# Optimization experiments

Hardware: AMD Instinct MI355X
Metric: run time of the kernel (lower is better)

## Reference

```python
import jax, jax.numpy as jnp
import numpy as np

EPS = 1e-5
ROPE_BASE = 10000.0


def _layernorm(x, g, b):
    mu = jnp.mean(x, axis=-1, keepdims=True)
    var = jnp.mean(jnp.square(x - mu), axis=-1, keepdims=True)
    return (x - mu) * jax.lax.rsqrt(var + EPS) * g + b


def _rope(q, k):
    # q, k: (B, T, H, D); rotate interleaved pairs along last dim, positions over T
    T, D = q.shape[1], q.shape[-1]
    half = D // 2
    inv_freq = ROPE_BASE ** (-jnp.arange(half, dtype=jnp.float32) / half)
    ang = jnp.arange(T, dtype=jnp.float32)[:, None] * inv_freq  # (T, half)
    cos = jnp.cos(ang)[None, :, None, :]
    sin = jnp.sin(ang)[None, :, None, :]

    def rot(x):
        xr, xi = x[..., 0::2], x[..., 1::2]
        yr = xr * cos - xi * sin
        yi = xr * sin + xi * cos
        return jnp.stack([yr, yi], axis=-1).reshape(x.shape)

    return rot(q), rot(k)


def setup_inputs() -> dict:
    key = jax.random.key(0)
    ks = jax.random.split(key, 5)
    E, F, B, T = 1024, 4096, 2, 2048
    s = 0.02
    return {
        "x": jax.random.normal(ks[0], (B, T, E), jnp.float32),
        "in_proj_w": jax.random.normal(ks[1], (3 * E, E), jnp.float32) * s,
        "out_proj_w": jax.random.normal(ks[2], (E, E), jnp.float32) * s,
        "ln1_g": jnp.ones((E,), jnp.float32),
        "ln1_b": jnp.zeros((E,), jnp.float32),
        "ln2_g": jnp.ones((E,), jnp.float32),
        "ln2_b": jnp.zeros((E,), jnp.float32),
        "w1": jax.random.normal(ks[3], (F, E), jnp.float32) * s,
        "w2": jax.random.normal(ks[4], (E, F), jnp.float32) * s,
        "context": 256,
    }


def reference(x, in_proj_w, out_proj_w, ln1_g, ln1_b, ln2_g, ln2_b, w1, w2, context):
    B, T, E = x.shape
    H = 16
    D = E // H

    # ---- self-attention block (pre-norm, residual) ----
    h = _layernorm(x, ln1_g, ln1_b)
    proj = h @ in_proj_w.T  # (B, T, 3E)
    qkv = proj.reshape(B, T, 3, H, D)
    q = qkv[:, :, 0]  # (B, T, H, D)
    k = qkv[:, :, 1]
    v = qkv[:, :, 2].transpose(0, 2, 1, 3)  # (B, H, T, D)
    q, k = _rope(q, k)
    q = q.transpose(0, 2, 1, 3)  # (B, H, T, D)
    k = k.transpose(0, 2, 1, 3)

    pos = jnp.arange(T)
    delta = pos[:, None] - pos[None, :]  # (T, T)
    mask = (delta >= 0) & (delta < context)

    scores = jnp.einsum("bhtd,bhsd->bhts", q, k) / jnp.sqrt(jnp.float32(D))
    scores = jnp.where(mask[None, None], scores, jnp.float32(-1e30))
    attn = jax.nn.softmax(scores, axis=-1)
    o = jnp.einsum("bhts,bhsd->bhtd", attn, v)
    o = o.transpose(0, 2, 1, 3).reshape(B, T, E)
    x = x + o @ out_proj_w.T

    # ---- FFN block (pre-norm, residual) ----
    h = _layernorm(x, ln2_g, ln2_b)
    update = jax.nn.gelu(h @ w1.T, approximate=False) @ w2.T
    return x + update
```

## Files before the change

### kernel.cpp

```cpp
#include <hip/hip_runtime.h>
#include <math.h>

#define B_BATCH 2
#define T_SEQ   2048
#define E_DIM   1024
#define H_HEADS 16
#define D_HEAD  64
#define F_DIM   4096
#define M_ROWS  (B_BATCH * T_SEQ)

typedef __attribute__((ext_vector_type(8))) short short8;
typedef __attribute__((ext_vector_type(4))) float floatx4;
typedef __attribute__((ext_vector_type(8))) unsigned short ushortx8;

typedef __attribute__((address_space(1))) const void global_cvoid;
typedef __attribute__((address_space(3))) void lds_void;

__device__ __forceinline__ unsigned short f2bf(float f) {
    unsigned u = __float_as_uint(f);
    u += 0x7fffu + ((u >> 16) & 1u);
    return (unsigned short)(u >> 16);
}
__device__ __forceinline__ float bf2f(unsigned short h) {
    return __uint_as_float(((unsigned)h) << 16);
}

__device__ __forceinline__ float gelu_f(float v) {
    const float u = v * (0.7978845608f + 0.0356774081f * v * v);
    const float e = __expf(2.0f * u);
    const float t = 1.0f - 2.0f / (e + 1.0f);
    return 0.5f * v * (1.0f + t);
}

__device__ __forceinline__ float waveReduceSum(float v) {
#pragma unroll
    for (int off = 32; off > 0; off >>= 1) v += __shfl_xor(v, off, 64);
    return v;
}

__global__ __launch_bounds__(256) void cvt_all_kernel(const float* __restrict__ ipw,
                                                      const float* __restrict__ opw,
                                                      const float* __restrict__ w1,
                                                      const float* __restrict__ w2,
                                                      unsigned short* __restrict__ wqkv,
                                                      unsigned short* __restrict__ wout,
                                                      unsigned short* __restrict__ w1b,
                                                      unsigned short* __restrict__ w2b) {
    const size_t MEG = 1024u * 1024u;
    size_t i = ((size_t)blockIdx.x * 256 + threadIdx.x) * 4;
    const float* src;
    unsigned short* dst;
    size_t off;
    if (i < 3 * MEG)      { src = ipw; dst = wqkv; off = i; }
    else if (i < 4 * MEG) { src = opw; dst = wout; off = i - 3 * MEG; }
    else if (i < 8 * MEG) { src = w1;  dst = w1b;  off = i - 4 * MEG; }
    else                  { src = w2;  dst = w2b;  off = i - 8 * MEG; }
    float4 v = *(const float4*)(src + off);
    ushort4 o;
    o.x = f2bf(v.x); o.y = f2bf(v.y); o.z = f2bf(v.z); o.w = f2bf(v.w);
    *(ushort4*)(dst + off) = o;
}

template <bool HASR>
__global__ __launch_bounds__(256) void reduce4_kernel(const unsigned short* __restrict__ p,
                                                      const float* __restrict__ R,
                                                      float* __restrict__ out, int n) {
    const int i = (blockIdx.x * 256 + threadIdx.x) * 8;
    if (i >= n) return;
    ushortx8 a0 = *(const ushortx8*)(p + i);
    ushortx8 a1 = *(const ushortx8*)(p + (size_t)n + i);
    ushortx8 a2 = *(const ushortx8*)(p + 2 * (size_t)n + i);
    ushortx8 a3 = *(const ushortx8*)(p + 3 * (size_t)n + i);
    float base[8];
    if (HASR) {
        float4 r0 = *(const float4*)(R + i);
        float4 r1 = *(const float4*)(R + i + 4);
        base[0]=r0.x; base[1]=r0.y; base[2]=r0.z; base[3]=r0.w;
        base[4]=r1.x; base[5]=r1.y; base[6]=r1.z; base[7]=r1.w;
    } else {
        float4 r0 = *(const float4*)(out + i);
        float4 r1 = *(const float4*)(out + i + 4);
        base[0]=r0.x; base[1]=r0.y; base[2]=r0.z; base[3]=r0.w;
        base[4]=r1.x; base[5]=r1.y; base[6]=r1.z; base[7]=r1.w;
    }
    float4 o0, o1;
    float* op = &o0.x;
#pragma unroll
    for (int j = 0; j < 8; ++j) {
        float s = base[j] + (bf2f(a0[j]) + bf2f(a1[j])) + (bf2f(a2[j]) + bf2f(a3[j]));
        if (j < 4) (&o0.x)[j] = s; else (&o1.x)[j - 4] = s;
    }
    (void)op;
    *(float4*)(out + i)     = o0;
    *(float4*)(out + i + 4) = o1;
}

__global__ __launch_bounds__(256) void rope_tab_kernel(float* __restrict__ tab) {
    const int idx = blockIdx.x * 256 + threadIdx.x;
    const int pos = idx >> 5, i = idx & 31;
    const float invf = powf(10000.0f, -(float)i / 32.0f);
    const float ang = (float)pos * invf;
    tab[idx * 2]     = cosf(ang);
    tab[idx * 2 + 1] = sinf(ang);
}

__global__ __launch_bounds__(256) void ln_kernel(const float* __restrict__ x,
                                                 const float* __restrict__ g,
                                                 const float* __restrict__ b,
                                                 unsigned short* __restrict__ out) {
    const int row = blockIdx.x;
    const float* xr = x + (size_t)row * E_DIM;
    float4 v = ((const float4*)xr)[threadIdx.x];
    float s  = v.x + v.y + v.z + v.w;
    float sq = v.x * v.x + v.y * v.y + v.z * v.z + v.w * v.w;

    __shared__ float red[8];
    float ws_ = waveReduceSum(s);
    float wq  = waveReduceSum(sq);
    int wid = threadIdx.x >> 6;
    if ((threadIdx.x & 63) == 0) { red[wid] = ws_; red[wid + 4] = wq; }
    __syncthreads();
    float ts = red[0] + red[1] + red[2] + red[3];
    float tq = red[4] + red[5] + red[6] + red[7];
    float mean = ts * (1.0f / E_DIM);
    float var  = tq * (1.0f / E_DIM) - mean * mean;
    float inv  = rsqrtf(var + 1e-5f);

    float4 gv = ((const float4*)g)[threadIdx.x];
    float4 bv = ((const float4*)b)[threadIdx.x];
    ushort4 o;
    o.x = f2bf((v.x - mean) * inv * gv.x + bv.x);
    o.y = f2bf((v.y - mean) * inv * gv.y + bv.y);
    o.z = f2bf((v.z - mean) * inv * gv.z + bv.z);
    o.w = f2bf((v.w - mean) * inv * gv.w + bv.w);
    ((ushort4*)(out + (size_t)row * E_DIM))[threadIdx.x] = o;
}

template <int EPI, int Z>
__global__ __launch_bounds__(256) void gemm_bf16(const unsigned short* __restrict__ A,
                                                 const unsigned short* __restrict__ Wt,
                                                 float* __restrict__ Cf,
                                                 unsigned short* __restrict__ Cb,
                                                 int M, int N, int K) {
    __shared__ unsigned short As[128 * 64];
    __shared__ unsigned short Bs[128 * 64];
    const int tid  = threadIdx.x;
    const int wave = tid >> 6, lane = tid & 63;
    const int wm   = wave >> 1, wn = wave & 1;
    const int quad = lane >> 4, l16 = lane & 15;

    const int id  = blockIdx.x;
    const int xcd = id & 7, local = id >> 3;
    const int mq  = M >> 9;
    const int mt  = (xcd & 3) + 4 * (local % mq);
    int nt_, zz;
    if (Z == 1) {
        zz  = 0;
        nt_ = (xcd >> 2) + 2 * (local / mq);
    } else {
        zz  = (xcd >> 2) + 2 * ((local / mq) & 1);
        nt_ = local / (mq * 2);
    }
    const int m0 = mt * 128, n0 = nt_ * 128;
    const int Kc = K / Z, kbeg = zz * Kc;

    const int row_rel = lane >> 3;
    const int ch      = lane & 7;

    const floatx4 z = {0.0f, 0.0f, 0.0f, 0.0f};
    floatx4 acc[4][4];
#pragma unroll
    for (int i = 0; i < 4; ++i)
#pragma unroll
        for (int j = 0; j < 4; ++j) acc[i][j] = z;

    for (int k0 = kbeg; k0 < kbeg + Kc; k0 += 64) {
        __syncthreads();
#pragma unroll
        for (int i = 0; i < 4; ++i) {
            const int chunk = wave * 4 + i;
            const int grow  = chunk * 8 + row_rel;
            const int lch   = ch ^ (grow & 7);
            const unsigned short* ga = A  + (size_t)(m0 + grow) * K + k0 + lch * 8;
            const unsigned short* gb = Wt + (size_t)(n0 + grow) * K + k0 + lch * 8;
            __builtin_amdgcn_global_load_lds((global_cvoid*)ga,
                                             (lds_void*)(As + chunk * 512), 16, 0, 0);
            __builtin_amdgcn_global_load_lds((global_cvoid*)gb,
                                             (lds_void*)(Bs + chunk * 512), 16, 0, 0);
        }
        __syncthreads();

#pragma unroll
        for (int ks = 0; ks < 2; ++ks) {
            short8 af[4], bfr[4];
#pragma unroll
            for (int mt2 = 0; mt2 < 4; ++mt2) {
                const int r = wm * 64 + mt2 * 16 + l16;
                const int p = (ks * 4 + quad) ^ (r & 7);
                af[mt2] = *(const short8*)(As + r * 64 + p * 8);
            }
#pragma unroll
            for (int nt2 = 0; nt2 < 4; ++nt2) {
                const int r = wn * 64 + nt2 * 16 + l16;
                const int p = (ks * 4 + quad) ^ (r & 7);
                bfr[nt2] = *(const short8*)(Bs + r * 64 + p * 8);
            }
#pragma unroll
            for (int mt2 = 0; mt2 < 4; ++mt2)
#pragma unroll
                for (int nt2 = 0; nt2 < 4; ++nt2)
                    acc[mt2][nt2] = __builtin_amdgcn_mfma_f32_16x16x32_bf16(
                        af[mt2], bfr[nt2], acc[mt2][nt2], 0, 0, 0);
        }
    }

    const size_t zoff = (size_t)zz * M * N;
#pragma unroll
    for (int mt2 = 0; mt2 < 4; ++mt2) {
        const int rb = m0 + wm * 64 + mt2 * 16 + quad * 4;
#pragma unroll
        for (int nt2 = 0; nt2 < 4; ++nt2) {
            const int col = n0 + wn * 64 + nt2 * 16 + l16;
#pragma unroll
            for (int r = 0; r < 4; ++r) {
                const size_t idx = (size_t)(rb + r) * N + col;
                const float v = acc[mt2][nt2][r];
                if (EPI == 2) {
                    Cb[idx] = f2bf(gelu_f(v));
                } else if (EPI == 4) {
                    Cb[idx] = f2bf(v);
                } else {
                    Cb[zoff + idx] = f2bf(v);
                }
            }
        }
    }
}

__global__ __launch_bounds__(256) void vtrans_kernel(const unsigned short* __restrict__ proj,
                                                     unsigned short* __restrict__ vt) {
    __shared__ unsigned short L[64 * 72];
    const int bh = blockIdx.y, b = bh >> 4, h = bh & 15;
    const int st = blockIdx.x * 64;
    const int tid = threadIdx.x;
    {
        const int srel = tid >> 2, d16 = (tid & 3) * 16;
        const unsigned short* src =
            proj + (size_t)(b * T_SEQ + st + srel) * (3 * E_DIM) + 2 * E_DIM + h * 64 + d16;
        *(short8*)(L + srel * 72 + d16)     = *(const short8*)(src);
        *(short8*)(L + srel * 72 + d16 + 8) = *(const short8*)(src + 8);
    }
    __syncthreads();
    {
        const int d = tid >> 2, s16 = (tid & 3) * 16;
        short8 o0, o1;
#pragma unroll
        for (int j = 0; j < 8; ++j) {
            o0[j] = (short)L[(s16 + j) * 72 + d];
            o1[j] = (short)L[(s16 + 8 + j) * 72 + d];
        }
        unsigned short* dst = vt + (size_t)(bh * 64 + d) * T_SEQ + st + s16;
        *(short8*)dst       = o0;
        *(short8*)(dst + 8) = o1;
    }
}

__device__ __forceinline__ void rope16(ushortx8 x0, ushortx8 x1, const float* tp,
                                       short8& y0, short8& y1) {
#pragma unroll
    for (int j = 0; j < 4; ++j) {
        const float c = tp[2 * j], s = tp[2 * j + 1];
        const float xr = bf2f(x0[2 * j]), xi = bf2f(x0[2 * j + 1]);
        y0[2 * j]     = (short)f2bf(xr * c - xi * s);
        y0[2 * j + 1] = (short)f2bf(xr * s + xi * c);
    }
#pragma unroll
    for (int j = 0; j < 4; ++j) {
        const float c = tp[8 + 2 * j], s = tp[8 + 2 * j + 1];
        const float xr = bf2f(x1[2 * j]), xi = bf2f(x1[2 * j + 1]);
        y1[2 * j]     = (short)f2bf(xr * c - xi * s);
        y1[2 * j + 1] = (short)f2bf(xr * s + xi * c);
    }
}

__global__ __launch_bounds__(256) void attn_kernel(const unsigned short* __restrict__ proj,
                                                   const unsigned short* __restrict__ vt,
                                                   const float* __restrict__ tab,
                                                   const int* __restrict__ ctxp,
                                                   unsigned short* __restrict__ o) {
    __shared__ unsigned short Qs[64 * 64];
    __shared__ unsigned short Ks[64 * 64];
    __shared__ unsigned short Vs[64 * 64];
    __shared__ unsigned short Ps[4][16 * 64];

    const int ctx = ctxp[0];
    const int tid = threadIdx.x;
    const int wave = tid >> 6, lane = tid & 63;
    const int quad = lane >> 4, l16 = lane & 15;
    const int bh = blockIdx.y, b = bh >> 4, h = bh & 15;
    const int t0 = blockIdx.x * 64;

    {
        const int r = tid >> 2, d16 = (tid & 3) * 16;
        const int pos = t0 + r;
        const unsigned short* src =
            proj + (size_t)(b * T_SEQ + pos) * (3 * E_DIM) + h * 64 + d16;
        ushortx8 x0 = *(const ushortx8*)src;
        ushortx8 x1 = *(const ushortx8*)(src + 8);
        const float* tp = tab + ((size_t)pos * 32 + (d16 >> 1)) * 2;
        short8 y0, y1;
        rope16(x0, x1, tp, y0, y1);
        const int c0 = (tid & 3) * 2;
        *(short8*)(Qs + r * 64 + ((c0)     ^ (r & 7)) * 8) = y0;
        *(short8*)(Qs + r * 64 + ((c0 + 1) ^ (r & 7)) * 8) = y1;
    }

    int first = t0 - (ctx - 1);
    if (first < 0) first = 0;
    const int first_base = first & ~63;

    float m[4] = {-1e30f, -1e30f, -1e30f, -1e30f};
    float l[4] = {0.0f, 0.0f, 0.0f, 0.0f};
    const floatx4 z = {0.0f, 0.0f, 0.0f, 0.0f};
    floatx4 accO[4] = {z, z, z, z};

    const int q_row0 = t0 + wave * 16 + quad * 4;

    for (int s_base = first_base; s_base <= t0; s_base += 64) {
        __syncthreads();
        {
            const int r = tid >> 2, d16 = (tid & 3) * 16;
            const int pos = s_base + r;
            const unsigned short* src =
                proj + (size_t)(b * T_SEQ + pos) * (3 * E_DIM) + E_DIM + h * 64 + d16;
            ushortx8 x0 = *(const ushortx8*)src;
            ushortx8 x1 = *(const ushortx8*)(src + 8);
            const float* tp = tab + ((size_t)pos * 32 + (d16 >> 1)) * 2;
            short8 y0, y1;
            rope16(x0, x1, tp, y0, y1);
            const int c0 = (tid & 3) * 2;
            *(short8*)(Ks + r * 64 + ((c0)     ^ (r & 7)) * 8) = y0;
            *(short8*)(Ks + r * 64 + ((c0 + 1) ^ (r & 7)) * 8) = y1;
        }
#pragma unroll
        for (int i = 0; i < 2; ++i) {
            const int chunk = (wave * 2 + i) * 64 + lane;
            const int d = chunk >> 3, c = chunk & 7;
            const unsigned short* gsrc =
                vt + (size_t)(bh * 64 + d) * T_SEQ + s_base + ((c ^ (d & 7)) * 8);
            __builtin_amdgcn_global_load_lds((global_cvoid*)gsrc,
                                             (lds_void*)(Vs + (wave * 2 + i) * 512),
                                             16, 0, 0);
        }
        __syncthreads();

        floatx4 accS[4] = {z, z, z, z};
#pragma unroll
        for (int ks = 0; ks < 2; ++ks) {
            const int qrow = wave * 16 + l16;
            short8 aq = *(const short8*)(Qs + qrow * 64 + (((ks * 4 + quad) ^ (qrow & 7)) * 8));
#pragma unroll
            for (int nt = 0; nt < 4; ++nt) {
                const int kro = nt * 16 + l16;
                short8 bk = *(const short8*)(Ks + kro * 64 + (((ks * 4 + quad) ^ (kro & 7)) * 8));
                accS[nt] = __builtin_amdgcn_mfma_f32_16x16x32_bf16(aq, bk, accS[nt], 0, 0, 0);
            }
        }

        float p[4][4];
        float alpha[4];
#pragma unroll
        for (int r = 0; r < 4; ++r) {
            const int qa = q_row0 + r;
            float sv[4];
            float vmax = -1e30f;
#pragma unroll
            for (int nt = 0; nt < 4; ++nt) {
                const int sa = s_base + nt * 16 + l16;
                const int dd = qa - sa;
                const bool ok = (unsigned)dd < (unsigned)ctx;
                const float s = ok ? accS[nt][r] * 0.125f : -1e30f;
                sv[nt] = s;
                vmax = fmaxf(vmax, s);
            }
            vmax = fmaxf(vmax, __shfl_xor(vmax, 1));
            vmax = fmaxf(vmax, __shfl_xor(vmax, 2));
            vmax = fmaxf(vmax, __shfl_xor(vmax, 4));
            vmax = fmaxf(vmax, __shfl_xor(vmax, 8));
            const float mn = fmaxf(m[r], vmax);
            alpha[r] = __expf(m[r] - mn);
            float ps = 0.0f;
#pragma unroll
            for (int nt = 0; nt < 4; ++nt) {
                const float pe = (sv[nt] > -0.5e30f) ? __expf(sv[nt] - mn) : 0.0f;
                p[nt][r] = pe;
                ps += pe;
            }
            ps += __shfl_xor(ps, 1);
            ps += __shfl_xor(ps, 2);
            ps += __shfl_xor(ps, 4);
            ps += __shfl_xor(ps, 8);
            l[r] = l[r] * alpha[r] + ps;
            m[r] = mn;
        }

#pragma unroll
        for (int nt = 0; nt < 4; ++nt) {
#pragma unroll
            for (int r = 0; r < 4; ++r) {
                const int row = quad * 4 + r;
                const int col = nt * 16 + l16;
                Ps[wave][row * 64 + (((col >> 3) ^ (row & 7)) * 8) + (col & 7)] =
                    f2bf(p[nt][r]);
            }
        }
#pragma unroll
        for (int nt = 0; nt < 4; ++nt)
#pragma unroll
            for (int r = 0; r < 4; ++r) accO[nt][r] *= alpha[r];

#pragma unroll
        for (int ks = 0; ks < 2; ++ks) {
            short8 ap = *(const short8*)(&Ps[wave][l16 * 64 + (((ks * 4 + quad) ^ (l16 & 7)) * 8)]);
#pragma unroll
            for (int nt = 0; nt < 4; ++nt) {
                const int dr = nt * 16 + l16;
                short8 bv = *(const short8*)(Vs + dr * 64 + (((ks * 4 + quad) ^ (dr & 7)) * 8));
                accO[nt] = __builtin_amdgcn_mfma_f32_16x16x32_bf16(ap, bv, accO[nt], 0, 0, 0);
            }
        }
    }

    float inv[4];
#pragma unroll
    for (int r = 0; r < 4; ++r) inv[r] = 1.0f / l[r];
#pragma unroll
    for (int nt = 0; nt < 4; ++nt) {
#pragma unroll
        for (int r = 0; r < 4; ++r) {
            const int t = q_row0 + r;
            o[(size_t)(b * T_SEQ + t) * E_DIM + h * 64 + nt * 16 + l16] =
                f2bf(accO[nt][r] * inv[r]);
        }
    }
}

extern "C" void kernel_launch(void* const* d_in, const int* in_sizes, int n_in,
                              void* d_out, int out_size, void* d_ws, size_t ws_size,
                              hipStream_t stream) {
    const float* x          = (const float*)d_in[0];
    const float* in_proj_w  = (const float*)d_in[1];
    const float* out_proj_w = (const float*)d_in[2];
    const float* ln1_g      = (const float*)d_in[3];
    const float* ln1_b      = (const float*)d_in[4];
    const float* ln2_g      = (const float*)d_in[5];
    const float* ln2_b      = (const float*)d_in[6];
    const float* w1         = (const float*)d_in[7];
    const float* w2         = (const float*)d_in[8];
    const int*   ctx        = (const int*)d_in[9];
    float* out = (float*)d_out;
    float* ws  = (float*)d_ws;

    const size_t MEG = 1024u * 1024u;
    unsigned short* u = (unsigned short*)ws;
    unsigned short* w2_b   = u;
    unsigned short* wqkv_b = u + 4 * MEG;
    unsigned short* wout_b = u + 7 * MEG;
    unsigned short* w1_b   = u + 8 * MEG;
    unsigned short* h_b    = u + 12 * MEG;
    unsigned short* obuf_b = u + 16 * MEG;
    unsigned short* proj_b = u + 20 * MEG;
    unsigned short* vt_b   = u + 32 * MEG;
    unsigned short* mid_b  = u + 36 * MEG;
    float* tab  = ws + 26 * MEG;
    unsigned short* part_op   = u + 20 * MEG;
    unsigned short* part_mlp2 = u + 4 * MEG;

    cvt_all_kernel<<<12 * MEG / 1024, 256, 0, stream>>>(
        in_proj_w, out_proj_w, w1, w2, wqkv_b, wout_b, w1_b, w2_b);
    rope_tab_kernel<<<T_SEQ * 32 / 256, 256, 0, stream>>>(tab);

    ln_kernel<<<M_ROWS, 256, 0, stream>>>(x, ln1_g, ln1_b, h_b);
    gemm_bf16<4, 1><<<32 * 24, 256, 0, stream>>>(
        h_b, wqkv_b, nullptr, proj_b, M_ROWS, 3 * E_DIM, E_DIM);
    vtrans_kernel<<<dim3(T_SEQ / 64, B_BATCH * H_HEADS), 256, 0, stream>>>(proj_b, vt_b);
    attn_kernel<<<dim3(T_SEQ / 64, B_BATCH * H_HEADS), 256, 0, stream>>>(
        proj_b, vt_b, tab, ctx, obuf_b);
    gemm_bf16<5, 4><<<32 * 8 * 4, 256, 0, stream>>>(
        obuf_b, wout_b, nullptr, part_op, M_ROWS, E_DIM, E_DIM);
    reduce4_kernel<true><<<M_ROWS * E_DIM / 2048, 256, 0, stream>>>(
        part_op, x, out, M_ROWS * E_DIM);
    ln_kernel<<<M_ROWS, 256, 0, stream>>>(out, ln2_g, ln2_b, h_b);
    gemm_bf16<2, 1><<<32 * 32, 256, 0, stream>>>(
        h_b, w1_b, nullptr, mid_b, M_ROWS, F_DIM, E_DIM);
    gemm_bf16<5, 4><<<32 * 8 * 4, 256, 0, stream>>>(
        mid_b, w2_b, nullptr, part_mlp2, M_ROWS, E_DIM, F_DIM);
    reduce4_kernel<false><<<M_ROWS * E_DIM / 2048, 256, 0, stream>>>(
        part_mlp2, nullptr, out, M_ROWS * E_DIM);
}
```

Baseline: 337.8 us.

## Fuse V transpose into QKV GEMM epilogue and residual-reduce into LayerNorm

```diff
diff --git a/kernel.cpp b/kernel.cpp
--- a/kernel.cpp
+++ b/kernel.cpp
@@ -61,40 +61,6 @@
     *(ushort4*)(dst + off) = o;
 }
 
-template <bool HASR>
-__global__ __launch_bounds__(256) void reduce4_kernel(const unsigned short* __restrict__ p,
-                                                      const float* __restrict__ R,
-                                                      float* __restrict__ out, int n) {
-    const int i = (blockIdx.x * 256 + threadIdx.x) * 8;
-    if (i >= n) return;
-    ushortx8 a0 = *(const ushortx8*)(p + i);
-    ushortx8 a1 = *(const ushortx8*)(p + (size_t)n + i);
-    ushortx8 a2 = *(const ushortx8*)(p + 2 * (size_t)n + i);
-    ushortx8 a3 = *(const ushortx8*)(p + 3 * (size_t)n + i);
-    float base[8];
-    if (HASR) {
-        float4 r0 = *(const float4*)(R + i);
-        float4 r1 = *(const float4*)(R + i + 4);
-        base[0]=r0.x; base[1]=r0.y; base[2]=r0.z; base[3]=r0.w;
-        base[4]=r1.x; base[5]=r1.y; base[6]=r1.z; base[7]=r1.w;
-    } else {
-        float4 r0 = *(const float4*)(out + i);
-        float4 r1 = *(const float4*)(out + i + 4);
-        base[0]=r0.x; base[1]=r0.y; base[2]=r0.z; base[3]=r0.w;
-        base[4]=r1.x; base[5]=r1.y; base[6]=r1.z; base[7]=r1.w;
-    }
-    float4 o0, o1;
-    float* op = &o0.x;
-#pragma unroll
-    for (int j = 0; j < 8; ++j) {
-        float s = base[j] + (bf2f(a0[j]) + bf2f(a1[j])) + (bf2f(a2[j]) + bf2f(a3[j]));
-        if (j < 4) (&o0.x)[j] = s; else (&o1.x)[j - 4] = s;
-    }
-    (void)op;
-    *(float4*)(out + i)     = o0;
-    *(float4*)(out + i + 4) = o1;
-}
-
 __global__ __launch_bounds__(256) void rope_tab_kernel(float* __restrict__ tab) {
     const int idx = blockIdx.x * 256 + threadIdx.x;
     const int pos = idx >> 5, i = idx & 31;
@@ -136,10 +102,187 @@
     ((ushort4*)(out + (size_t)row * E_DIM))[threadIdx.x] = o;
 }
 
+__global__ __launch_bounds__(256) void reduce_ln_kernel(const unsigned short* __restrict__ p,
+                                                        const float* __restrict__ x,
+                                                        const float* __restrict__ g,
+                                                        const float* __restrict__ bb,
+                                                        float* __restrict__ out,
+                                                        unsigned short* __restrict__ h) {
+    const int tid = threadIdx.x;
+    const int rh = tid >> 7;
+    const int l128 = tid & 127;
+    const int row = blockIdx.x * 2 + rh;
+    const size_t base = (size_t)row * E_DIM + l128 * 8;
+    const size_t n = (size_t)M_ROWS * E_DIM;
+
+    ushortx8 a0 = *(const ushortx8*)(p + base);
+    ushortx8 a1 = *(const ushortx8*)(p + n + base);
+    ushortx8 a2 = *(const ushortx8*)(p + 2 * n + base);
+    ushortx8 a3 = *(const ushortx8*)(p + 3 * n + base);
+    float4 r0 = *(const float4*)(x + base);
+    float4 r1 = *(const float4*)(x + base + 4);
+    float s[8] = {r0.x, r0.y, r0.z, r0.w, r1.x, r1.y, r1.z, r1.w};
+    float sum = 0.0f, sq = 0.0f;
+#pragma unroll
+    for (int j = 0; j < 8; ++j) {
+        s[j] += (bf2f(a0[j]) + bf2f(a1[j])) + (bf2f(a2[j]) + bf2f(a3[j]));
+        sum += s[j];
+        sq  += s[j] * s[j];
+    }
+    float4 o0 = {s[0], s[1], s[2], s[3]}, o1 = {s[4], s[5], s[6], s[7]};
+    *(float4*)(out + base)     = o0;
+    *(float4*)(out + base + 4) = o1;
+
+    sum = waveReduceSum(sum);
+    sq  = waveReduceSum(sq);
+    __shared__ float red[4][2];
+    const int wid = tid >> 6;
+    if ((tid & 63) == 0) { red[wid][0] = sum; red[wid][1] = sq; }
+    __syncthreads();
+    const float ts = red[rh * 2][0] + red[rh * 2 + 1][0];
+    const float tq = red[rh * 2][1] + red[rh * 2 + 1][1];
+    const float mean = ts * (1.0f / E_DIM);
+    const float var  = tq * (1.0f / E_DIM) - mean * mean;
+    const float inv  = rsqrtf(var + 1e-5f);
+
+    float4 g0 = *(const float4*)(g + l128 * 8);
+    float4 g1 = *(const float4*)(g + l128 * 8 + 4);
+    float4 b0 = *(const float4*)(bb + l128 * 8);
+    float4 b1 = *(const float4*)(bb + l128 * 8 + 4);
+    const float ga[8] = {g0.x, g0.y, g0.z, g0.w, g1.x, g1.y, g1.z, g1.w};
+    const float ba[8] = {b0.x, b0.y, b0.z, b0.w, b1.x, b1.y, b1.z, b1.w};
+    ushortx8 ho;
+#pragma unroll
+    for (int j = 0; j < 8; ++j) ho[j] = f2bf((s[j] - mean) * inv * ga[j] + ba[j]);
+    *(ushortx8*)(h + base) = ho;
+}
+
+__global__ __launch_bounds__(256) void reduce4_kernel(const unsigned short* __restrict__ p,
+                                                      float* __restrict__ out, int n) {
+    const int i = (blockIdx.x * 256 + threadIdx.x) * 8;
+    if (i >= n) return;
+    ushortx8 a0 = *(const ushortx8*)(p + i);
+    ushortx8 a1 = *(const ushortx8*)(p + (size_t)n + i);
+    ushortx8 a2 = *(const ushortx8*)(p + 2 * (size_t)n + i);
+    ushortx8 a3 = *(const ushortx8*)(p + 3 * (size_t)n + i);
+    float4 r0 = *(const float4*)(out + i);
+    float4 r1 = *(const float4*)(out + i + 4);
+    float s[8] = {r0.x, r0.y, r0.z, r0.w, r1.x, r1.y, r1.z, r1.w};
+#pragma unroll
+    for (int j = 0; j < 8; ++j)
+        s[j] += (bf2f(a0[j]) + bf2f(a1[j])) + (bf2f(a2[j]) + bf2f(a3[j]));
+    float4 o0 = {s[0], s[1], s[2], s[3]}, o1 = {s[4], s[5], s[6], s[7]};
+    *(float4*)(out + i)     = o0;
+    *(float4*)(out + i + 4) = o1;
+}
+
+__global__ __launch_bounds__(256) void gemm_qkv(const unsigned short* __restrict__ A,
+                                                const unsigned short* __restrict__ Wt,
+                                                unsigned short* __restrict__ proj,
+                                                unsigned short* __restrict__ vt) {
+    __shared__ unsigned short As[128 * 64];
+    __shared__ unsigned short Bs[128 * 64];
+    const int tid  = threadIdx.x;
+    const int wave = tid >> 6, lane = tid & 63;
+    const int wm   = wave >> 1, wn = wave & 1;
+    const int quad = lane >> 4, l16 = lane & 15;
+    const int M = M_ROWS, N = 3 * E_DIM, K = E_DIM;
+
+    const int id  = blockIdx.x;
+    const int xcd = id & 7, local = id >> 3;
+    const int mq  = M >> 9;
+    const int mt  = (xcd & 3) + 4 * (local % mq);
+    const int nt_ = (xcd >> 2) + 2 * (local / mq);
+    const int m0 = mt * 128, n0 = nt_ * 128;
+
+    const int row_rel = lane >> 3;
+    const int ch      = lane & 7;
+
+    const floatx4 z = {0.0f, 0.0f, 0.0f, 0.0f};
+    floatx4 acc[4][4];
+#pragma unroll
+    for (int i = 0; i < 4; ++i)
+#pragma unroll
+        for (int j = 0; j < 4; ++j) acc[i][j] = z;
+
+    for (int k0 = 0; k0 < K; k0 += 64) {
+        __syncthreads();
+#pragma unroll
+        for (int i = 0; i < 4; ++i) {
+            const int chunk = wave * 4 + i;
+            const int grow  = chunk * 8 + row_rel;
+            const int lch   = ch ^ (grow & 7);
+            const unsigned short* ga = A  + (size_t)(m0 + grow) * K + k0 + lch * 8;
+            const unsigned short* gb = Wt + (size_t)(n0 + grow) * K + k0 + lch * 8;
+            __builtin_amdgcn_global_load_lds((global_cvoid*)ga,
+                                             (lds_void*)(As + chunk * 512), 16, 0, 0);
+            __builtin_amdgcn_global_load_lds((global_cvoid*)gb,
+                                             (lds_void*)(Bs + chunk * 512), 16, 0, 0);
+        }
+        __syncthreads();
+
+#pragma unroll
+        for (int ks = 0; ks < 2; ++ks) {
+            short8 af[4], bfr[4];
+#pragma unroll
+            for (int mt2 = 0; mt2 < 4; ++mt2) {
+                const int r = wm * 64 + mt2 * 16 + l16;
+                const int p = (ks * 4 + quad) ^ (r & 7);
+                af[mt2] = *(const short8*)(As + r * 64 + p * 8);
+            }
+#pragma unroll
+            for (int nt2 = 0; nt2 < 4; ++nt2) {
+                const int r = wn * 64 + nt2 * 16 + l16;
+                const int p = (ks * 4 + quad) ^ (r & 7);
+                bfr[nt2] = *(const short8*)(Bs + r * 64 + p * 8);
+            }
+#pragma unroll
+            for (int mt2 = 0; mt2 < 4; ++mt2)
+#pragma unroll
+                for (int nt2 = 0; nt2 < 4; ++nt2)
+                    acc[mt2][nt2] = __builtin_amdgcn_mfma_f32_16x16x32_bf16(
+                        af[mt2], bfr[nt2], acc[mt2][nt2], 0, 0, 0);
+        }
+    }
+
+    const int type = n0 >> 10;
+    if (type < 2) {
+#pragma unroll
+        for (int mt2 = 0; mt2 < 4; ++mt2) {
+            const int rb = m0 + wm * 64 + mt2 * 16 + quad * 4;
+#pragma unroll
+            for (int nt2 = 0; nt2 < 4; ++nt2) {
+                const int col = n0 + wn * 64 + nt2 * 16 + l16;
+#pragma unroll
+                for (int r = 0; r < 4; ++r)
+                    proj[(size_t)(rb + r) * N + col] = f2bf(acc[mt2][nt2][r]);
+            }
+        }
+    } else {
+#pragma unroll
+        for (int mt2 = 0; mt2 < 4; ++mt2) {
+            const int rb = m0 + wm * 64 + mt2 * 16 + quad * 4;
+            const int t = rb & (T_SEQ - 1);
+            const int b = rb >> 11;
+#pragma unroll
+            for (int nt2 = 0; nt2 < 4; ++nt2) {
+                const int col = n0 + wn * 64 + nt2 * 16 + l16;
+                const int hh = (col - 2048) >> 6;
+                const int d  = col & 63;
+                ushort4 pk;
+                pk.x = f2bf(acc[mt2][nt2][0]);
+                pk.y = f2bf(acc[mt2][nt2][1]);
+                pk.z = f2bf(acc[mt2][nt2][2]);
+                pk.w = f2bf(acc[mt2][nt2][3]);
+                *(ushort4*)(vt + (((size_t)(b * H_HEADS + hh) * 64) + d) * T_SEQ + t) = pk;
+            }
+        }
+    }
+}
+
 template <int EPI, int Z>
 __global__ __launch_bounds__(256) void gemm_bf16(const unsigned short* __restrict__ A,
                                                  const unsigned short* __restrict__ Wt,
-                                                 float* __restrict__ Cf,
                                                  unsigned short* __restrict__ Cb,
                                                  int M, int N, int K) {
     __shared__ unsigned short As[128 * 64];
@@ -227,41 +370,11 @@
                 const float v = acc[mt2][nt2][r];
                 if (EPI == 2) {
                     Cb[idx] = f2bf(gelu_f(v));
-                } else if (EPI == 4) {
-                    Cb[idx] = f2bf(v);
                 } else {
                     Cb[zoff + idx] = f2bf(v);
                 }
             }
         }
-    }
-}
-
-__global__ __launch_bounds__(256) void vtrans_kernel(const unsigned short* __restrict__ proj,
-                                                     unsigned short* __restrict__ vt) {
-    __shared__ unsigned short L[64 * 72];
-    const int bh = blockIdx.y, b = bh >> 4, h = bh & 15;
-    const int st = blockIdx.x * 64;
-    const int tid = threadIdx.x;
-    {
-        const int srel = tid >> 2, d16 = (tid & 3) * 16;
-        const unsigned short* src =
-            proj + (size_t)(b * T_SEQ + st + srel) * (3 * E_DIM) + 2 * E_DIM + h * 64 + d16;
-        *(short8*)(L + srel * 72 + d16)     = *(const short8*)(src);
-        *(short8*)(L + srel * 72 + d16 + 8) = *(const short8*)(src + 8);
-    }
-    __syncthreads();
-    {
-        const int d = tid >> 2, s16 = (tid & 3) * 16;
-        short8 o0, o1;
-#pragma unroll
-        for (int j = 0; j < 8; ++j) {
-            o0[j] = (short)L[(s16 + j) * 72 + d];
-            o1[j] = (short)L[(s16 + 8 + j) * 72 + d];
-        }
-        unsigned short* dst = vt + (size_t)(bh * 64 + d) * T_SEQ + st + s16;
-        *(short8*)dst       = o0;
-        *(short8*)(dst + 8) = o1;
     }
 }
 
@@ -349,8 +462,7 @@
             const unsigned short* gsrc =
                 vt + (size_t)(bh * 64 + d) * T_SEQ + s_base + ((c ^ (d & 7)) * 8);
             __builtin_amdgcn_global_load_lds((global_cvoid*)gsrc,
-                                             (lds_void*)(Vs + (wave * 2 + i) * 512),
-                                             16, 0, 0);
+                                             (lds_void*)(Vs + (wave * 2 + i) * 512), 16, 0, 0);
         }
         __syncthreads();
 
@@ -472,7 +584,7 @@
     unsigned short* proj_b = u + 20 * MEG;
     unsigned short* vt_b   = u + 32 * MEG;
     unsigned short* mid_b  = u + 36 * MEG;
-    float* tab  = ws + 26 * MEG;
+    float* tab = ws + 26 * MEG;
     unsigned short* part_op   = u + 20 * MEG;
     unsigned short* part_mlp2 = u + 4 * MEG;
 
@@ -481,20 +593,17 @@
     rope_tab_kernel<<<T_SEQ * 32 / 256, 256, 0, stream>>>(tab);
 
     ln_kernel<<<M_ROWS, 256, 0, stream>>>(x, ln1_g, ln1_b, h_b);
-    gemm_bf16<4, 1><<<32 * 24, 256, 0, stream>>>(
-        h_b, wqkv_b, nullptr, proj_b, M_ROWS, 3 * E_DIM, E_DIM);
-    vtrans_kernel<<<dim3(T_SEQ / 64, B_BATCH * H_HEADS), 256, 0, stream>>>(proj_b, vt_b);
+    gemm_qkv<<<32 * 24, 256, 0, stream>>>(h_b, wqkv_b, proj_b, vt_b);
     attn_kernel<<<dim3(T_SEQ / 64, B_BATCH * H_HEADS), 256, 0, stream>>>(
         proj_b, vt_b, tab, ctx, obuf_b);
     gemm_bf16<5, 4><<<32 * 8 * 4, 256, 0, stream>>>(
-        obuf_b, wout_b, nullptr, part_op, M_ROWS, E_DIM, E_DIM);
-    reduce4_kernel<true><<<M_ROWS * E_DIM / 2048, 256, 0, stream>>>(
-        part_op, x, out, M_ROWS * E_DIM);
-    ln_kernel<<<M_ROWS, 256, 0, stream>>>(out, ln2_g, ln2_b, h_b);
+        obuf_b, wout_b, part_op, M_ROWS, E_DIM, E_DIM);
+    reduce_ln_kernel<<<M_ROWS / 2, 256, 0, stream>>>(
+        part_op, x, ln2_g, ln2_b, out, h_b);
     gemm_bf16<2, 1><<<32 * 32, 256, 0, stream>>>(
-        h_b, w1_b, nullptr, mid_b, M_ROWS, F_DIM, E_DIM);
+        h_b, w1_b, mid_b, M_ROWS, F_DIM, E_DIM);
     gemm_bf16<5, 4><<<32 * 8 * 4, 256, 0, stream>>>(
-        mid_b, w2_b, nullptr, part_mlp2, M_ROWS, E_DIM, F_DIM);
-    reduce4_kernel<false><<<M_ROWS * E_DIM / 2048, 256, 0, stream>>>(
-        part_mlp2, nullptr, out, M_ROWS * E_DIM);
-}
+        mid_b, w2_b, part_mlp2, M_ROWS, E_DIM, F_DIM);
+    reduce4_kernel<<<M_ROWS * E_DIM / 2048, 256, 0, stream>>>(
+        part_mlp2, out, M_ROWS * E_DIM);
+}
```

Result: no change. 337.6 us (-0.1%).
